# Kernel optimization log

Measured on AMD Instinct MI355X. Metric: run time of the kernel, lower is better.

Reference implementation:

```python
import math
import jax, jax.numpy as jnp
import numpy as np

B, M, L, H = 8, 2048, 2048, 1024


def setup_inputs() -> dict:
    key = jax.random.key(0)
    k1, k2, k3, k4 = jax.random.split(key, 4)
    return {
        "query": jax.random.normal(k1, (B, M, H), dtype=jnp.float32),
        "key": jax.random.normal(k2, (B, L, H), dtype=jnp.float32),
        "value": jax.random.normal(k3, (B, L, H), dtype=jnp.float32),
        "key_pe": jax.random.normal(k4, (1, H, L), dtype=jnp.float32),
        "hidden_size": H,
    }


def reference(query, key, value, key_pe, hidden_size):
    # content scores: [B, M, L]
    attn_cont = jnp.einsum("bmh,blh->bml", query, key)
    # relative-position scores: [B, M, H] @ [1, H, L] -> [B, M, L]
    attn_pos = jnp.matmul(query, key_pe)
    # NOTE: the original module computes softmax(attn)+dropout but then
    # (as written) multiplies VALUE by the raw content scores, not the
    # softmaxed attention. We reproduce that math faithfully; the softmax
    # is dead code w.r.t. the output (kept here for documentation, DCE'd by jit).
    attn = jax.nn.softmax((attn_cont + attn_pos) / math.sqrt(hidden_size), axis=-1)  # noqa: F841
    # dropout: identity in eval mode (and unused for the output anyway)
    out = jnp.matmul(attn_cont, value)  # [B, M, H]
    return out
```

## Files before the change

### kernel.cpp

```cpp
#include <hip/hip_runtime.h>
#include <hip/hip_bf16.h>


typedef __bf16 bf16x8 __attribute__((ext_vector_type(8)));
typedef float f32x4 __attribute__((ext_vector_type(4)));
typedef unsigned short u16_t;

#define GLD_LDS16(g, l)                                                        \
  __builtin_amdgcn_global_load_lds(                                            \
      (const __attribute__((address_space(1))) void*)(g),                      \
      (__attribute__((address_space(3))) void*)(l), 16, 0, 0)

static __device__ inline u16_t f2b(float x) {
  __hip_bfloat16 h = __float2bfloat16(x);
  u16_t u;
  __builtin_memcpy(&u, &h, 2);
  return u;
}

__global__ __launch_bounds__(256) void cvt_f32_bf16(
    const float* __restrict__ in, u16_t* __restrict__ out, size_t n8) {
  const size_t i = (size_t)blockIdx.x * 256 + threadIdx.x;
  if (i >= n8) return;
  const float4 a = *(const float4*)(in + i * 8);
  const float4 b = *(const float4*)(in + i * 8 + 4);
  u16_t v[8] = {f2b(a.x), f2b(a.y), f2b(a.z), f2b(a.w),
                f2b(b.x), f2b(b.y), f2b(b.z), f2b(b.w)};
  *(uint4*)(out + i * 8) = *(const uint4*)v;
}

__global__ __launch_bounds__(256) void transpose_cvt(
    const float* __restrict__ in, u16_t* __restrict__ out, int L, int Hd) {
  __shared__ u16_t tile[64 * 65];
  in  += (size_t)blockIdx.z * (size_t)L * Hd;
  out += (size_t)blockIdx.z * (size_t)L * Hd;
  const int h0 = blockIdx.x * 64;
  const int l0 = blockIdx.y * 64;

  const int c4 = (threadIdx.x & 15) * 4;
  const int r0 = threadIdx.x >> 4;
#pragma unroll
  for (int it = 0; it < 4; ++it) {
    const int r = r0 + 16 * it;
    const float4 f = *(const float4*)(in + (size_t)(l0 + r) * Hd + h0 + c4);
    tile[(c4 + 0) * 65 + r] = f2b(f.x);
    tile[(c4 + 1) * 65 + r] = f2b(f.y);
    tile[(c4 + 2) * 65 + r] = f2b(f.z);
    tile[(c4 + 3) * 65 + r] = f2b(f.w);
  }
  __syncthreads();

  const int c8 = (threadIdx.x & 7) * 8;
  const int rr = threadIdx.x >> 3;
#pragma unroll
  for (int it = 0; it < 2; ++it) {
    const int r = rr + 32 * it;
    u16_t p[8];
#pragma unroll
    for (int u = 0; u < 8; ++u) p[u] = tile[r * 65 + c8 + u];
    *(uint4*)(out + (size_t)(h0 + r) * L + l0 + c8) = *(const uint4*)p;
  }
}

static __device__ inline void store_c(float* p, float v) { *p = v; }
static __device__ inline void store_c(u16_t* p, float v) { *p = f2b(v); }

template <typename OutT>
__global__ __launch_bounds__(256) void gemm_bt_128(
    const u16_t* __restrict__ A, const u16_t* __restrict__ Bt,
    OutT* __restrict__ C, int M, int N, int K, long sA, long sB, long sC) {
  __shared__ __align__(16) u16_t As[128 * 64];
  __shared__ __align__(16) u16_t Bs[128 * 64];

  const int batch = blockIdx.x & 7;
  const int t = blockIdx.x >> 3;
  const int m0 = (t >> 3) * 128;
  const int n0 = (t & 7) * 128;

  A  += (size_t)batch * (size_t)sA;
  Bt += (size_t)batch * (size_t)sB;
  C  += (size_t)batch * (size_t)sC;

  const int tid = threadIdx.x;
  const int lane = tid & 63;
  const int w  = tid >> 6;
  const int wm = w & 1;
  const int wn = w >> 1;
  const int s  = lane & 15;
  const int q  = lane >> 4;

  const u16_t* gA[4];
  const u16_t* gB[4];
  u16_t* lA[4];
  u16_t* lB[4];
#pragma unroll
  for (int j = 0; j < 4; ++j) {
    const int i = tid + 256 * j;
    const int row = i >> 3;
    const int gchunk = (i & 7) ^ (row & 7);
    gA[j] = A  + (size_t)(m0 + row) * K + gchunk * 8;
    gB[j] = Bt + (size_t)(n0 + row) * K + gchunk * 8;
    lA[j] = As + i * 8;
    lB[j] = Bs + i * 8;
  }

  f32x4 acc[4][4];
#pragma unroll
  for (int r = 0; r < 4; ++r)
#pragma unroll
    for (int c = 0; c < 4; ++c) acc[r][c] = (f32x4){0.f, 0.f, 0.f, 0.f};

  const int s7 = s & 7;

  for (int k0 = 0; k0 < K; k0 += 64) {
#pragma unroll
    for (int j = 0; j < 4; ++j) {
      GLD_LDS16(gA[j] + k0, lA[j]);
      GLD_LDS16(gB[j] + k0, lB[j]);
    }
    __syncthreads();

#pragma unroll
    for (int kk = 0; kk < 2; ++kk) {
      const int slot = (kk * 4 + q) ^ s7;
      bf16x8 af[4], bfr[4];
#pragma unroll
      for (int r = 0; r < 4; ++r)
        af[r] = *(const bf16x8*)(As + (64 * wm + 16 * r + s) * 64 + slot * 8);
#pragma unroll
      for (int c = 0; c < 4; ++c)
        bfr[c] = *(const bf16x8*)(Bs + (64 * wn + 16 * c + s) * 64 + slot * 8);
#pragma unroll
      for (int r = 0; r < 4; ++r)
#pragma unroll
        for (int c = 0; c < 4; ++c)
          acc[r][c] = __builtin_amdgcn_mfma_f32_16x16x32_bf16(af[r], bfr[c],
                                                              acc[r][c], 0, 0, 0);
    }
    __syncthreads();
  }

#pragma unroll
  for (int r = 0; r < 4; ++r) {
#pragma unroll
    for (int c = 0; c < 4; ++c) {
      const int col = n0 + 64 * wn + 16 * c + s;
#pragma unroll
      for (int e = 0; e < 4; ++e) {
        const int row = m0 + 64 * wm + 16 * r + q * 4 + e;
        store_c(&C[(size_t)row * N + col], acc[r][c][e]);
      }
    }
  }
}

extern "C" void kernel_launch(void* const* d_in, const int* in_sizes, int n_in,
                              void* d_out, int out_size, void* d_ws, size_t ws_size,
                              hipStream_t stream) {
  const int B = 8, M = 2048, L = 2048, H = 1024;

  const float* q = (const float*)d_in[0];
  const float* k = (const float*)d_in[1];
  const float* v = (const float*)d_in[2];

  const size_t nKt = (size_t)B * H * L;
  const size_t nQ  = (size_t)B * M * H;
  const size_t nW  = (size_t)B * H * H;
  const size_t need = (2 * nKt + nQ + nW) * sizeof(u16_t);
  if (ws_size < need) return;

  u16_t* Kt = (u16_t*)d_ws;
  u16_t* Vt = Kt + nKt;
  u16_t* Qb = Vt + nKt;
  u16_t* W  = Qb + nQ;

  dim3 tb(256);

  cvt_f32_bf16<<<dim3((unsigned)(nQ / 8 / 256)), tb, 0, stream>>>(q, Qb, nQ / 8);

  dim3 tg(H / 64, L / 64, B);
  transpose_cvt<<<tg, tb, 0, stream>>>(k, Kt, L, H);
  transpose_cvt<<<tg, tb, 0, stream>>>(v, Vt, L, H);

  gemm_bt_128<u16_t><<<dim3(B * (H / 128) * (H / 128)), tb, 0, stream>>>(
      Vt, Kt, W, H, H, L, (long)H * L, (long)H * L, (long)H * H);

  gemm_bt_128<float><<<dim3(B * (M / 128) * (H / 128)), tb, 0, stream>>>(
      Qb, W, (float*)d_out, M, H, H, (long)M * H, (long)H * H, (long)M * H);
}
```

Before: 315.1 us.

## Fuse Q bf16 conversion into second GEMM and merge K/V transposes

Drops the separate Q fp32-to-bf16 conversion kernel. The second GEMM now loads fp32 Q directly from global memory, converts it in registers and writes bf16 into LDS. The K and V transpose-convert kernels are merged into one launch, and the LDS tile now holds packed bf16 pairs, giving wider shared-memory stores and reads. This removes a round trip of the Q buffer through memory and two launches. In exchange the A-operand load in the GEMM is now synchronous through registers instead of an async global-to-LDS copy, and it reads twice the bytes per tile.

```diff
diff --git a/kernel.cpp b/kernel.cpp
--- a/kernel.cpp
+++ b/kernel.cpp
@@ -17,49 +17,46 @@
   __builtin_memcpy(&u, &h, 2);
   return u;
 }
-
-__global__ __launch_bounds__(256) void cvt_f32_bf16(
-    const float* __restrict__ in, u16_t* __restrict__ out, size_t n8) {
-  const size_t i = (size_t)blockIdx.x * 256 + threadIdx.x;
-  if (i >= n8) return;
-  const float4 a = *(const float4*)(in + i * 8);
-  const float4 b = *(const float4*)(in + i * 8 + 4);
-  u16_t v[8] = {f2b(a.x), f2b(a.y), f2b(a.z), f2b(a.w),
-                f2b(b.x), f2b(b.y), f2b(b.z), f2b(b.w)};
-  *(uint4*)(out + i * 8) = *(const uint4*)v;
-}
-
-__global__ __launch_bounds__(256) void transpose_cvt(
-    const float* __restrict__ in, u16_t* __restrict__ out, int L, int Hd) {
-  __shared__ u16_t tile[64 * 65];
-  in  += (size_t)blockIdx.z * (size_t)L * Hd;
-  out += (size_t)blockIdx.z * (size_t)L * Hd;
+static __device__ inline unsigned pack2(float a, float b) {
+  return (unsigned)f2b(a) | ((unsigned)f2b(b) << 16);
+}
+
+__global__ __launch_bounds__(256) void transpose_cvt2(
+    const float* __restrict__ Kin, const float* __restrict__ Vin,
+    u16_t* __restrict__ Kt, u16_t* __restrict__ Vt, int L, int Hd) {
+  __shared__ unsigned tile[64 * 33];
+  const int bz = blockIdx.z;
+  const float* in = (bz < 8) ? Kin : Vin;
+  u16_t* out = (bz < 8) ? Kt : Vt;
+  const int batch = bz & 7;
+  in  += (size_t)batch * (size_t)L * Hd;
+  out += (size_t)batch * (size_t)L * Hd;
   const int h0 = blockIdx.x * 64;
   const int l0 = blockIdx.y * 64;
 
-  const int c4 = (threadIdx.x & 15) * 4;
-  const int r0 = threadIdx.x >> 4;
-#pragma unroll
-  for (int it = 0; it < 4; ++it) {
-    const int r = r0 + 16 * it;
-    const float4 f = *(const float4*)(in + (size_t)(l0 + r) * Hd + h0 + c4);
-    tile[(c4 + 0) * 65 + r] = f2b(f.x);
-    tile[(c4 + 1) * 65 + r] = f2b(f.y);
-    tile[(c4 + 2) * 65 + r] = f2b(f.z);
-    tile[(c4 + 3) * 65 + r] = f2b(f.w);
+  const int h4 = (threadIdx.x & 15) * 4;
+  const int lp0 = threadIdx.x >> 4;
+#pragma unroll
+  for (int it = 0; it < 2; ++it) {
+    const int lp = lp0 + 16 * it;
+    const int l = 2 * lp;
+    const float4 f0 = *(const float4*)(in + (size_t)(l0 + l) * Hd + h0 + h4);
+    const float4 f1 = *(const float4*)(in + (size_t)(l0 + l + 1) * Hd + h0 + h4);
+    tile[(h4 + 0) * 33 + lp] = pack2(f0.x, f1.x);
+    tile[(h4 + 1) * 33 + lp] = pack2(f0.y, f1.y);
+    tile[(h4 + 2) * 33 + lp] = pack2(f0.z, f1.z);
+    tile[(h4 + 3) * 33 + lp] = pack2(f0.w, f1.w);
   }
   __syncthreads();
 
-  const int c8 = (threadIdx.x & 7) * 8;
-  const int rr = threadIdx.x >> 3;
-#pragma unroll
-  for (int it = 0; it < 2; ++it) {
-    const int r = rr + 32 * it;
-    u16_t p[8];
-#pragma unroll
-    for (int u = 0; u < 8; ++u) p[u] = tile[r * 65 + c8 + u];
-    *(uint4*)(out + (size_t)(h0 + r) * L + l0 + c8) = *(const uint4*)p;
-  }
+  const int h = threadIdx.x >> 2;
+  const int half = threadIdx.x & 3;
+  unsigned u[8];
+#pragma unroll
+  for (int j = 0; j < 8; ++j) u[j] = tile[h * 33 + 8 * half + j];
+  u16_t* dst = out + (size_t)(h0 + h) * L + l0 + 16 * half;
+  *(uint4*)(dst)     = *(const uint4*)(u);
+  *(uint4*)(dst + 8) = *(const uint4*)(u + 4);
 }
 
 static __device__ inline void store_c(float* p, float v) { *p = v; }
@@ -154,6 +151,106 @@
   }
 }
 
+__global__ __launch_bounds__(256) void gemm2_qf32(
+    const float* __restrict__ Af, const u16_t* __restrict__ Bt,
+    float* __restrict__ C, int M, int N, int K, long sA, long sB, long sC) {
+  __shared__ __align__(16) u16_t As[128 * 64];
+  __shared__ __align__(16) u16_t Bs[128 * 64];
+
+  const int batch = blockIdx.x & 7;
+  const int t = blockIdx.x >> 3;
+  const int m0 = (t >> 3) * 128;
+  const int n0 = (t & 7) * 128;
+
+  Af += (size_t)batch * (size_t)sA;
+  Bt += (size_t)batch * (size_t)sB;
+  C  += (size_t)batch * (size_t)sC;
+
+  const int tid = threadIdx.x;
+  const int lane = tid & 63;
+  const int w  = tid >> 6;
+  const int wm = w & 1;
+  const int wn = w >> 1;
+  const int s  = lane & 15;
+  const int q  = lane >> 4;
+
+  const float* gA[4];
+  const u16_t* gB[4];
+  uint4* lA[4];
+  u16_t* lB[4];
+#pragma unroll
+  for (int j = 0; j < 4; ++j) {
+    const int i = tid + 256 * j;
+    const int row = i >> 3;
+    const int gchunk = (i & 7) ^ (row & 7);
+    gA[j] = Af + (size_t)(m0 + row) * K + gchunk * 8;
+    gB[j] = Bt + (size_t)(n0 + row) * K + gchunk * 8;
+    lA[j] = (uint4*)(As + i * 8);
+    lB[j] = Bs + i * 8;
+  }
+
+  f32x4 acc[4][4];
+#pragma unroll
+  for (int r = 0; r < 4; ++r)
+#pragma unroll
+    for (int c = 0; c < 4; ++c) acc[r][c] = (f32x4){0.f, 0.f, 0.f, 0.f};
+
+  const int s7 = s & 7;
+
+  for (int k0 = 0; k0 < K; k0 += 64) {
+#pragma unroll
+    for (int j = 0; j < 4; ++j) GLD_LDS16(gB[j] + k0, lB[j]);
+    float4 f0[4], f1[4];
+#pragma unroll
+    for (int j = 0; j < 4; ++j) {
+      f0[j] = *(const float4*)(gA[j] + k0);
+      f1[j] = *(const float4*)(gA[j] + k0 + 4);
+    }
+#pragma unroll
+    for (int j = 0; j < 4; ++j) {
+      uint4 wv;
+      wv.x = pack2(f0[j].x, f0[j].y);
+      wv.y = pack2(f0[j].z, f0[j].w);
+      wv.z = pack2(f1[j].x, f1[j].y);
+      wv.w = pack2(f1[j].z, f1[j].w);
+      *lA[j] = wv;
+    }
+    __syncthreads();
+
+#pragma unroll
+    for (int kk = 0; kk < 2; ++kk) {
+      const int slot = (kk * 4 + q) ^ s7;
+      bf16x8 af[4], bfr[4];
+#pragma unroll
+      for (int r = 0; r < 4; ++r)
+        af[r] = *(const bf16x8*)(As + (64 * wm + 16 * r + s) * 64 + slot * 8);
+#pragma unroll
+      for (int c = 0; c < 4; ++c)
+        bfr[c] = *(const bf16x8*)(Bs + (64 * wn + 16 * c + s) * 64 + slot * 8);
+#pragma unroll
+      for (int r = 0; r < 4; ++r)
+#pragma unroll
+        for (int c = 0; c < 4; ++c)
+          acc[r][c] = __builtin_amdgcn_mfma_f32_16x16x32_bf16(af[r], bfr[c],
+                                                              acc[r][c], 0, 0, 0);
+    }
+    __syncthreads();
+  }
+
+#pragma unroll
+  for (int r = 0; r < 4; ++r) {
+#pragma unroll
+    for (int c = 0; c < 4; ++c) {
+      const int col = n0 + 64 * wn + 16 * c + s;
+#pragma unroll
+      for (int e = 0; e < 4; ++e) {
+        const int row = m0 + 64 * wm + 16 * r + q * 4 + e;
+        C[(size_t)row * N + col] = acc[r][c][e];
+      }
+    }
+  }
+}
+
 extern "C" void kernel_launch(void* const* d_in, const int* in_sizes, int n_in,
                               void* d_out, int out_size, void* d_ws, size_t ws_size,
                               hipStream_t stream) {
@@ -164,27 +261,21 @@
   const float* v = (const float*)d_in[2];
 
   const size_t nKt = (size_t)B * H * L;
-  const size_t nQ  = (size_t)B * M * H;
   const size_t nW  = (size_t)B * H * H;
-  const size_t need = (2 * nKt + nQ + nW) * sizeof(u16_t);
+  const size_t need = (2 * nKt + nW) * sizeof(u16_t);
   if (ws_size < need) return;
 
   u16_t* Kt = (u16_t*)d_ws;
   u16_t* Vt = Kt + nKt;
-  u16_t* Qb = Vt + nKt;
-  u16_t* W  = Qb + nQ;
+  u16_t* W  = Vt + nKt;
 
   dim3 tb(256);
 
-  cvt_f32_bf16<<<dim3((unsigned)(nQ / 8 / 256)), tb, 0, stream>>>(q, Qb, nQ / 8);
-
-  dim3 tg(H / 64, L / 64, B);
-  transpose_cvt<<<tg, tb, 0, stream>>>(k, Kt, L, H);
-  transpose_cvt<<<tg, tb, 0, stream>>>(v, Vt, L, H);
+  transpose_cvt2<<<dim3(H / 64, L / 64, 2 * B), tb, 0, stream>>>(k, v, Kt, Vt, L, H);
 
   gemm_bt_128<u16_t><<<dim3(B * (H / 128) * (H / 128)), tb, 0, stream>>>(
       Vt, Kt, W, H, H, L, (long)H * L, (long)H * L, (long)H * H);
 
-  gemm_bt_128<float><<<dim3(B * (M / 128) * (H / 128)), tb, 0, stream>>>(
-      Qb, W, (float*)d_out, M, H, H, (long)M * H, (long)H * H, (long)M * H);
-}
+  gemm2_qf32<<<dim3(B * (M / 128) * (H / 128)), tb, 0, stream>>>(
+      q, W, (float*)d_out, M, H, H, (long)M * H, (long)H * H, (long)M * H);
+}
```

Result: no change. 316.6 us (+0.5%).

## Split-K the VᵀK GEMM, fuse K/V transposes and merge Q convert with partial sum

Applied to the files above, without the earlier changes.

The two K/V transpose-convert launches become one kernel, and the bf16 pair packing changes to 32-bit LDS entries. The first GEMM (Vt·Ktᵀ, K=2048) is split in two along K, giving 1024 blocks instead of 512 to fill more CUs. It writes two bf16 partial W buffers, which a combined kernel sums while also converting Q to bf16. Workspace is reused for Qb and Wb, so fewer launches and less memory are needed. The trade-off is extra W traffic and a second rounding of W to bf16.

```diff
diff --git a/kernel.cpp b/kernel.cpp
--- a/kernel.cpp
+++ b/kernel.cpp
@@ -17,69 +17,75 @@
   __builtin_memcpy(&u, &h, 2);
   return u;
 }
-
-__global__ __launch_bounds__(256) void cvt_f32_bf16(
-    const float* __restrict__ in, u16_t* __restrict__ out, size_t n8) {
-  const size_t i = (size_t)blockIdx.x * 256 + threadIdx.x;
-  if (i >= n8) return;
-  const float4 a = *(const float4*)(in + i * 8);
-  const float4 b = *(const float4*)(in + i * 8 + 4);
-  u16_t v[8] = {f2b(a.x), f2b(a.y), f2b(a.z), f2b(a.w),
-                f2b(b.x), f2b(b.y), f2b(b.z), f2b(b.w)};
-  *(uint4*)(out + i * 8) = *(const uint4*)v;
-}
-
-__global__ __launch_bounds__(256) void transpose_cvt(
-    const float* __restrict__ in, u16_t* __restrict__ out, int L, int Hd) {
-  __shared__ u16_t tile[64 * 65];
-  in  += (size_t)blockIdx.z * (size_t)L * Hd;
-  out += (size_t)blockIdx.z * (size_t)L * Hd;
+static __device__ inline unsigned pack2(float a, float b) {
+  return (unsigned)f2b(a) | ((unsigned)f2b(b) << 16);
+}
+static __device__ inline float b2f(u16_t u) {
+  unsigned v = (unsigned)u << 16;
+  float f;
+  __builtin_memcpy(&f, &v, 4);
+  return f;
+}
+
+__global__ __launch_bounds__(256) void transpose_kv(
+    const float* __restrict__ Kin, const float* __restrict__ Vin,
+    u16_t* __restrict__ Kt, u16_t* __restrict__ Vt, int L, int Hd) {
+  __shared__ unsigned tile[64 * 33];
+  const int bz = blockIdx.z;
+  const float* in = (bz < 8) ? Kin : Vin;
+  u16_t* out = (bz < 8) ? Kt : Vt;
+  const int batch = bz & 7;
+  in  += (size_t)batch * (size_t)L * Hd;
+  out += (size_t)batch * (size_t)L * Hd;
   const int h0 = blockIdx.x * 64;
   const int l0 = blockIdx.y * 64;
 
-  const int c4 = (threadIdx.x & 15) * 4;
-  const int r0 = threadIdx.x >> 4;
-#pragma unroll
-  for (int it = 0; it < 4; ++it) {
-    const int r = r0 + 16 * it;
-    const float4 f = *(const float4*)(in + (size_t)(l0 + r) * Hd + h0 + c4);
-    tile[(c4 + 0) * 65 + r] = f2b(f.x);
-    tile[(c4 + 1) * 65 + r] = f2b(f.y);
-    tile[(c4 + 2) * 65 + r] = f2b(f.z);
-    tile[(c4 + 3) * 65 + r] = f2b(f.w);
+  const int h4 = (threadIdx.x & 15) * 4;
+  const int lp0 = threadIdx.x >> 4;
+#pragma unroll
+  for (int it = 0; it < 2; ++it) {
+    const int lp = lp0 + 16 * it;
+    const int l = 2 * lp;
+    const float4 f0 = *(const float4*)(in + (size_t)(l0 + l) * Hd + h0 + h4);
+    const float4 f1 = *(const float4*)(in + (size_t)(l0 + l + 1) * Hd + h0 + h4);
+    tile[(h4 + 0) * 33 + lp] = pack2(f0.x, f1.x);
+    tile[(h4 + 1) * 33 + lp] = pack2(f0.y, f1.y);
+    tile[(h4 + 2) * 33 + lp] = pack2(f0.z, f1.z);
+    tile[(h4 + 3) * 33 + lp] = pack2(f0.w, f1.w);
   }
   __syncthreads();
 
-  const int c8 = (threadIdx.x & 7) * 8;
-  const int rr = threadIdx.x >> 3;
-#pragma unroll
-  for (int it = 0; it < 2; ++it) {
-    const int r = rr + 32 * it;
-    u16_t p[8];
-#pragma unroll
-    for (int u = 0; u < 8; ++u) p[u] = tile[r * 65 + c8 + u];
-    *(uint4*)(out + (size_t)(h0 + r) * L + l0 + c8) = *(const uint4*)p;
-  }
+  const int h = threadIdx.x >> 2;
+  const int half = threadIdx.x & 3;
+  unsigned u[8];
+#pragma unroll
+  for (int j = 0; j < 8; ++j) u[j] = tile[h * 33 + 8 * half + j];
+  u16_t* dst = out + (size_t)(h0 + h) * L + l0 + 16 * half;
+  *(uint4*)(dst)     = *(const uint4*)(u);
+  *(uint4*)(dst + 8) = *(const uint4*)(u + 4);
 }
 
 static __device__ inline void store_c(float* p, float v) { *p = v; }
 static __device__ inline void store_c(u16_t* p, float v) { *p = f2b(v); }
 
 template <typename OutT>
-__global__ __launch_bounds__(256) void gemm_bt_128(
+static __device__ inline void gemm_bt_body(
     const u16_t* __restrict__ A, const u16_t* __restrict__ Bt,
-    OutT* __restrict__ C, int M, int N, int K, long sA, long sB, long sC) {
+    OutT* __restrict__ C, int N, int K, int ldA, int ldB,
+    long sA, long sB, long sC, int tile_shift, long sCsplit) {
   __shared__ __align__(16) u16_t As[128 * 64];
   __shared__ __align__(16) u16_t Bs[128 * 64];
 
   const int batch = blockIdx.x & 7;
-  const int t = blockIdx.x >> 3;
-  const int m0 = (t >> 3) * 128;
-  const int n0 = (t & 7) * 128;
-
-  A  += (size_t)batch * (size_t)sA;
-  Bt += (size_t)batch * (size_t)sB;
-  C  += (size_t)batch * (size_t)sC;
+  const unsigned u = blockIdx.x >> 3;
+  const int kh = (int)(u >> tile_shift);
+  const unsigned t = u & ((1u << tile_shift) - 1u);
+  const int m0 = (int)(t >> 3) * 128;
+  const int n0 = (int)(t & 7) * 128;
+
+  A  += (size_t)batch * (size_t)sA + (size_t)kh * (size_t)K;
+  Bt += (size_t)batch * (size_t)sB + (size_t)kh * (size_t)K;
+  C  += (size_t)batch * (size_t)sC + (size_t)kh * (size_t)sCsplit;
 
   const int tid = threadIdx.x;
   const int lane = tid & 63;
@@ -98,8 +104,8 @@
     const int i = tid + 256 * j;
     const int row = i >> 3;
     const int gchunk = (i & 7) ^ (row & 7);
-    gA[j] = A  + (size_t)(m0 + row) * K + gchunk * 8;
-    gB[j] = Bt + (size_t)(n0 + row) * K + gchunk * 8;
+    gA[j] = A  + (size_t)(m0 + row) * ldA + gchunk * 8;
+    gB[j] = Bt + (size_t)(n0 + row) * ldB + gchunk * 8;
     lA[j] = As + i * 8;
     lB[j] = Bs + i * 8;
   }
@@ -154,6 +160,51 @@
   }
 }
 
+__global__ __launch_bounds__(256) void gemm1_kv(
+    const u16_t* __restrict__ Vt, const u16_t* __restrict__ Kt,
+    u16_t* __restrict__ W0, int N, int K, int ld, long sA, long sB, long sC,
+    long sCsplit) {
+  gemm_bt_body<u16_t>(Vt, Kt, W0, N, K, ld, ld, sA, sB, sC, 6, sCsplit);
+}
+
+__global__ __launch_bounds__(256) void gemm2_qw(
+    const u16_t* __restrict__ Qb, const u16_t* __restrict__ Wb,
+    float* __restrict__ C, int N, int K, long sA, long sB, long sC) {
+  gemm_bt_body<float>(Qb, Wb, C, N, K, K, K, sA, sB, sC, 7, 0);
+}
+
+__global__ __launch_bounds__(256) void qcvt_wsum(
+    const float* __restrict__ Q, const u16_t* __restrict__ W0,
+    const u16_t* __restrict__ W1, u16_t* __restrict__ Qb,
+    u16_t* __restrict__ Wb, size_t nQbatch, size_t nWbatch) {
+  const int batch = blockIdx.y;
+  if (blockIdx.z == 0) {
+    const size_t base = (size_t)batch * nQbatch +
+                        (size_t)blockIdx.x * 4096 + threadIdx.x * 16;
+    const float* src = Q + base;
+    u16_t* dst = Qb + base;
+#pragma unroll
+    for (int half = 0; half < 2; ++half) {
+      const float4 a = *(const float4*)(src + half * 8);
+      const float4 b = *(const float4*)(src + half * 8 + 4);
+      unsigned o[4] = {pack2(a.x, a.y), pack2(a.z, a.w),
+                       pack2(b.x, b.y), pack2(b.z, b.w)};
+      *(uint4*)(dst + half * 8) = *(const uint4*)o;
+    }
+  } else {
+    const size_t base = (size_t)batch * nWbatch +
+                        (size_t)blockIdx.x * 2048 + threadIdx.x * 8;
+    const uint4 u0 = *(const uint4*)(W0 + base);
+    const uint4 u1 = *(const uint4*)(W1 + base);
+    const u16_t* p0 = (const u16_t*)&u0;
+    const u16_t* p1 = (const u16_t*)&u1;
+    u16_t o[8];
+#pragma unroll
+    for (int j = 0; j < 8; ++j) o[j] = f2b(b2f(p0[j]) + b2f(p1[j]));
+    *(uint4*)(Wb + base) = *(const uint4*)o;
+  }
+}
+
 extern "C" void kernel_launch(void* const* d_in, const int* in_sizes, int n_in,
                               void* d_out, int out_size, void* d_ws, size_t ws_size,
                               hipStream_t stream) {
@@ -164,27 +215,28 @@
   const float* v = (const float*)d_in[2];
 
   const size_t nKt = (size_t)B * H * L;
-  const size_t nQ  = (size_t)B * M * H;
   const size_t nW  = (size_t)B * H * H;
-  const size_t need = (2 * nKt + nQ + nW) * sizeof(u16_t);
+  const size_t need = (2 * nKt + 2 * nW) * sizeof(u16_t);
   if (ws_size < need) return;
 
   u16_t* Kt = (u16_t*)d_ws;
   u16_t* Vt = Kt + nKt;
-  u16_t* Qb = Vt + nKt;
-  u16_t* W  = Qb + nQ;
+  u16_t* W0 = Vt + nKt;
+  u16_t* W1 = W0 + nW;
+  u16_t* Qb = Kt;
+  u16_t* Wb = Vt;
 
   dim3 tb(256);
 
-  cvt_f32_bf16<<<dim3((unsigned)(nQ / 8 / 256)), tb, 0, stream>>>(q, Qb, nQ / 8);
-
-  dim3 tg(H / 64, L / 64, B);
-  transpose_cvt<<<tg, tb, 0, stream>>>(k, Kt, L, H);
-  transpose_cvt<<<tg, tb, 0, stream>>>(v, Vt, L, H);
-
-  gemm_bt_128<u16_t><<<dim3(B * (H / 128) * (H / 128)), tb, 0, stream>>>(
-      Vt, Kt, W, H, H, L, (long)H * L, (long)H * L, (long)H * H);
-
-  gemm_bt_128<float><<<dim3(B * (M / 128) * (H / 128)), tb, 0, stream>>>(
-      Qb, W, (float*)d_out, M, H, H, (long)M * H, (long)H * H, (long)M * H);
-}
+  transpose_kv<<<dim3(H / 64, L / 64, 2 * B), tb, 0, stream>>>(k, v, Kt, Vt, L, H);
+
+  gemm1_kv<<<dim3(B * 64 * 2), tb, 0, stream>>>(
+      Vt, Kt, W0, H, L / 2, L, (long)H * L, (long)H * L, (long)H * H,
+      (long)B * H * H);
+
+  qcvt_wsum<<<dim3(512, B, 2), tb, 0, stream>>>(
+      q, W0, W1, Qb, Wb, (size_t)M * H, (size_t)H * H);
+
+  gemm2_qw<<<dim3(B * 128), tb, 0, stream>>>(
+      Qb, Wb, (float*)d_out, H, H, (long)M * H, (long)H * H, (long)M * H);
+}
```

New measurement: 315.1 us. Within noise of the previous version (-0.0%).
